# Kernel tuning notes

Hardware: AMD Instinct MI355X
Metric: run time of the kernel (lower is better)

Reference implementation:

```python
import jax, jax.numpy as jnp
import numpy as np

ALPHA = 1.0
N_OUTER, H_OUTER = 2, 0.5    # round(time_1/step_size_1) Euler steps of size step_size_1
N_INNER, H_INNER = 4, 0.25   # round(time_2/step_size_2) Euler steps inside each CGP


def _conv1x1(x, w, b):
    # x: [B,C,N,L], w: [O,C], b: [O] -> [B,O,N,L]  (1x1 Conv2d)
    return jnp.einsum('oc,bcnl->bonl', w, x) + b[None, :, None, None]


def _norm_adj(a):
    # row-normalized A + I
    a = a + jnp.eye(a.shape[0], dtype=a.dtype)
    return a / a.sum(axis=1, keepdims=True)


def _cgp(x, a_norm, w, b):
    # continuous graph propagation: dx/dt = alpha * (A_norm x - x), Euler integrated
    for _ in range(N_INNER):
        ax = jnp.einsum('nm,bcml->bcnl', a_norm, x)
        x = x + H_INNER * ALPHA * (ax - x)
    return _conv1x1(x, w, b)


def setup_inputs() -> dict:
    key = jax.random.key(0)
    ks = jax.random.split(key, 8)
    B, L, N, C_IN = 16, 12, 2000, 2
    C, E, C_OUT = 32, 128, 12

    def w(k, o, c, s=0.05):
        return jax.random.normal(k, (o, c), jnp.float32) * s

    return {
        'x': jax.random.normal(ks[0], (B, L, N, C_IN), jnp.float32),
        'adj': jax.random.uniform(ks[1], (N, N), jnp.float32),
        'w_start': w(ks[2], C, C_IN), 'b_start': jnp.zeros((C,), jnp.float32),
        'w_g1': w(ks[3], C, C), 'b_g1': jnp.zeros((C,), jnp.float32),
        'w_g2': w(ks[4], C, C), 'b_g2': jnp.zeros((C,), jnp.float32),
        'w_e0': w(ks[5], E // 2, C), 'b_e0': jnp.zeros((E // 2,), jnp.float32),
        'w_e1': w(ks[6], E, E // 2), 'b_e1': jnp.zeros((E,), jnp.float32),
        'w_e2': w(ks[7], C_OUT, E), 'b_e2': jnp.zeros((C_OUT,), jnp.float32),
    }


def reference(x, adj, w_start, b_start, w_g1, b_g1, w_g2, b_g2,
              w_e0, b_e0, w_e1, b_e1, w_e2, b_e2):
    # x: [B, L, N, C_in] -> channels-first [B, C_in, N, L]
    h = jnp.swapaxes(x, -1, -3)
    h = _conv1x1(h, w_start, b_start)
    a1 = _norm_adj(adj)
    a2 = _norm_adj(adj.T)
    # outer Euler ODE over STBlock (dropout = identity in eval mode)
    for _ in range(N_OUTER):
        h = h + H_OUTER * (_cgp(h, a1, w_g1, b_g1) + _cgp(h, a2, w_g2, b_g2))
    # layer_norm over all non-batch dims, no affine
    mu = h.mean(axis=(1, 2, 3), keepdims=True)
    var = h.var(axis=(1, 2, 3), keepdims=True)
    h = (h - mu) / jnp.sqrt(var + 1e-5)
    h = jax.nn.relu(_conv1x1(h, w_e0, b_e0))
    h = jax.nn.relu(_conv1x1(h, w_e1, b_e1))
    h = _conv1x1(h, w_e2, b_e2)
    return jnp.swapaxes(h, -1, -3)  # [B, L, N, out_channels]
```

## Files before the change

kernel.cpp:

```cpp
#include <hip/hip_runtime.h>
#include <math.h>

#define NN 2000
#define NP 2048
#define NB 16
#define NL 12
#define KW 6144
#define SW 384
#define LNCNT 768000.0f

#define O_ROWS ((size_t)0)
#define O_COLS ((size_t)2048)
#define O_LN   ((size_t)4096)
#define O_CM   ((size_t)4224)
#define O_CV   ((size_t)4672)
#define SZH ((size_t)2097152)
#define R1  ((size_t)8192)
#define R2  (R1 + 4*SZH)
#define R3  (R2 + 4*SZH)
#define O_X   (R3 + 0)
#define O_XTH (R3 + 768000)
#define O_XTL (O_XTH + 393216)
#define O_YF  (O_XTL + 393216)
#define O_YTH (O_YF + 1572864)
#define O_YTL (O_YTH + 786432)
#define O_ZF  (O_YTL + 786432)
#define O_H   R1

typedef __attribute__((ext_vector_type(8))) short short8;
typedef __attribute__((ext_vector_type(4))) float f32x4;

__device__ __forceinline__ unsigned short f2bf(float f) {
  union { float f; unsigned u; } x; x.f = f;
  unsigned r = x.u + 0x7fff + ((x.u >> 16) & 1);
  return (unsigned short)(r >> 16);
}
__device__ __forceinline__ float bf2f(unsigned short b) {
  union { unsigned u; float f; } x; x.u = ((unsigned)b) << 16;
  return x.f;
}
__device__ __forceinline__ void gld16(const void* g, void* l) {
  __builtin_amdgcn_global_load_lds(
      (const __attribute__((address_space(1))) unsigned int*)g,
      (__attribute__((address_space(3))) unsigned int*)l, 16, 0, 0);
}

__device__ __forceinline__ float blockReduceSum(float v, float* sbuf) {
  #pragma unroll
  for (int off = 32; off > 0; off >>= 1) v += __shfl_down(v, off, 64);
  int wid = threadIdx.x >> 6, lane = threadIdx.x & 63;
  if (lane == 0) sbuf[wid] = v;
  __syncthreads();
  v = (threadIdx.x < 4) ? sbuf[threadIdx.x] : 0.f;
  if (threadIdx.x < 64) { v += __shfl_down(v, 2, 64); v += __shfl_down(v, 1, 64); }
  return v;
}

__global__ void k_rowsum(const float* __restrict__ adj, float* __restrict__ rows) {
  __shared__ float sb[4];
  int n = blockIdx.x;
  const float4* a4 = (const float4*)(adj + (size_t)n * NN);
  float s = 0.f;
  for (int t = threadIdx.x; t < NN / 4; t += 256) {
    float4 v = a4[t];
    s += v.x + v.y + v.z + v.w;
  }
  s = blockReduceSum(s, sb);
  if (threadIdx.x == 0) rows[n] = s + 1.0f;
}

__global__ void k_colsum(const float* __restrict__ adj, float* __restrict__ cols) {
  __shared__ float sb[4][64];
  int col = blockIdx.x * 64 + (threadIdx.x & 63);
  int rg = threadIdx.x >> 6;
  float s = 0.f;
  if (col < NN)
    for (int m = rg; m < NN; m += 4) s += adj[(size_t)m * NN + col];
  sb[rg][threadIdx.x & 63] = s;
  __syncthreads();
  if (rg == 0 && col < NN)
    cols[col] = sb[0][threadIdx.x] + sb[1][threadIdx.x] + sb[2][threadIdx.x] + sb[3][threadIdx.x] + 1.0f;
}

__global__ void k_buildM8(const float* __restrict__ adj, const float* __restrict__ rows,
                          const float* __restrict__ cols,
                          unsigned short* __restrict__ M1h, unsigned short* __restrict__ M1l,
                          unsigned short* __restrict__ M2h, unsigned short* __restrict__ M2l,
                          unsigned short* __restrict__ M1Th, unsigned short* __restrict__ M1Tl,
                          unsigned short* __restrict__ M2Th, unsigned short* __restrict__ M2Tl) {
  __shared__ float Ta[64][65];
  __shared__ float Tb[64][65];
  int r0 = blockIdx.y * 64, c0 = blockIdx.x * 64;
  for (int e = threadIdx.x; e < 4096; e += 256) {
    int i = e >> 6, j = e & 63;
    int rr = r0 + i, cc = c0 + j;
    Ta[i][j] = (rr < NN && cc < NN) ? adj[(size_t)rr * NN + cc] : 0.f;
    int rr2 = c0 + i, cc2 = r0 + j;
    Tb[i][j] = (rr2 < NN && cc2 < NN) ? adj[(size_t)rr2 * NN + cc2] : 0.f;
  }
  __syncthreads();
  for (int e = threadIdx.x; e < 4096; e += 256) {
    int i = e >> 6, j = e & 63;
    int n = r0 + i, m = c0 + j;
    bool in = (n < NN && m < NN);
    float d = (n == m) ? 1.f : 0.f;
    float v1 = 0.f, v2 = 0.f, v1t = 0.f, v2t = 0.f;
    if (in) {
      v1  = 0.75f * d + 0.25f * (Ta[i][j] + d) / rows[n];
      v2  = 0.75f * d + 0.25f * (Tb[j][i] + d) / cols[n];
      v1t = 0.75f * d + 0.25f * (Tb[j][i] + d) / rows[m];
      v2t = 0.75f * d + 0.25f * (Ta[i][j] + d) / cols[m];
    }
    size_t o = (size_t)n * NP + m;
    unsigned short h;
    h = f2bf(v1);  M1h[o]  = h; M1l[o]  = f2bf(v1  - bf2f(h));
    h = f2bf(v2);  M2h[o]  = h; M2l[o]  = f2bf(v2  - bf2f(h));
    h = f2bf(v1t); M1Th[o] = h; M1Tl[o] = f2bf(v1t - bf2f(h));
    h = f2bf(v2t); M2Th[o] = h; M2Tl[o] = f2bf(v2t - bf2f(h));
  }
}

__global__ void k_prep(const float* __restrict__ wS, const float* __restrict__ bS,
                       const float* __restrict__ G1, const float* __restrict__ bg1,
                       const float* __restrict__ G2, const float* __restrict__ bg2,
                       float* __restrict__ Cm, float* __restrict__ cvec) {
  __shared__ float A1[64], A2[64], u1[32], v2[32];
  int t = threadIdx.x;
  int c = t >> 1, ci = t & 1;
  Cm[t] = wS[c * 2 + ci];
  float a1 = 0.f, a2 = 0.f;
  for (int j = 0; j < 32; ++j) {
    a1 += G1[c * 32 + j] * wS[j * 2 + ci];
    a2 += G2[c * 32 + j] * wS[j * 2 + ci];
  }
  A1[t] = a1; A2[t] = a2;
  Cm[64 + t] = a1;
  Cm[128 + t] = a2;
  __syncthreads();
  float b11 = 0, b12 = 0, b21 = 0, b22 = 0;
  for (int j = 0; j < 32; ++j) {
    b11 += G1[c * 32 + j] * A1[j * 2 + ci];
    b12 += G1[c * 32 + j] * A2[j * 2 + ci];
    b21 += G2[c * 32 + j] * A1[j * 2 + ci];
    b22 += G2[c * 32 + j] * A2[j * 2 + ci];
  }
  Cm[192 + t] = 0.25f * b11;
  Cm[256 + t] = 0.25f * b12;
  Cm[320 + t] = 0.25f * b21;
  Cm[384 + t] = 0.25f * b22;
  if (t < 32) {
    float uu = 0.f, vv = 0.f;
    for (int j = 0; j < 32; ++j) {
      float F = G1[t * 32 + j] + G2[t * 32 + j];
      uu += F * bS[j];
      vv += F * (bg1[j] + bg2[j]);
    }
    u1[t] = uu; v2[t] = vv;
  }
  __syncthreads();
  if (t < 32) {
    float u2v = 0.f;
    for (int j = 0; j < 32; ++j)
      u2v += (G1[t * 32 + j] + G2[t * 32 + j]) * u1[j];
    cvec[t] = bS[t] + u1[t] + 0.25f * u2v + (bg1[t] + bg2[t]) + 0.25f * v2[t];
  }
}

struct MG {
  const unsigned short *ah, *al, *bh, *bl;
  unsigned short *ch, *cl;
  float *cf;
};

template <int BN_, int OUTF32>
__global__ __launch_bounds__(256) void mgemm(MG g0, MG g1, int lda, int ldb,
                                             int ldc, int K) {
  MG g = (blockIdx.z == 0) ? g0 : g1;
  __shared__ __align__(16) unsigned short sAh[128 * 32];
  __shared__ __align__(16) unsigned short sAl[128 * 32];
  __shared__ __align__(16) unsigned short sBh[BN_ * 32];
  __shared__ __align__(16) unsigned short sBl[BN_ * 32];
  const int tid = threadIdx.x;
  const int wid = tid >> 6, lane = tid & 63;
  const int row0 = blockIdx.y * 128, col0 = blockIdx.x * BN_;
  const int FN = BN_ / 32;
  const int wr = (wid >> 1) * 64;
  const int wc = (wid & 1) * (BN_ / 2);
  const int lr = lane & 15;
  const int lk = (lane >> 4) * 8;
  const int r16 = lane >> 2;
  const int k16 = (lane & 3) * 8;
  const int BCH = BN_ / 16;
  const int CPW = (16 + 2 * BCH) / 4;

  f32x4 acc[4][FN];
  #pragma unroll
  for (int m = 0; m < 4; ++m)
    #pragma unroll
    for (int n = 0; n < FN; ++n) acc[m][n] = {0.f, 0.f, 0.f, 0.f};

  for (int k0 = 0; k0 < K; k0 += 32) {
    #pragma unroll
    for (int c = 0; c < CPW; ++c) {
      int gch = wid * CPW + c;
      const unsigned short* src;
      unsigned short* dst;
      if (gch < 16) {
        int q = gch & 7;
        src = (gch < 8 ? g.ah : g.al) + (size_t)(row0 + q * 16 + r16) * lda + k0 + k16;
        dst = (gch < 8 ? sAh : sAl) + q * 512;
      } else {
        int gb = gch - 16;
        int q = (gb < BCH) ? gb : gb - BCH;
        src = (gb < BCH ? g.bh : g.bl) + (size_t)(col0 + q * 16 + r16) * ldb + k0 + k16;
        dst = (gb < BCH ? sBh : sBl) + q * 512;
      }
      gld16(src, dst);
    }
    __syncthreads();
    short8 ahf[4], alf[4], bhf[FN], blf[FN];
    #pragma unroll
    for (int m = 0; m < 4; ++m) {
      ahf[m] = *(const short8*)&sAh[(wr + m * 16 + lr) * 32 + lk];
      alf[m] = *(const short8*)&sAl[(wr + m * 16 + lr) * 32 + lk];
    }
    #pragma unroll
    for (int n = 0; n < FN; ++n) {
      bhf[n] = *(const short8*)&sBh[(wc + n * 16 + lr) * 32 + lk];
      blf[n] = *(const short8*)&sBl[(wc + n * 16 + lr) * 32 + lk];
    }
    #pragma unroll
    for (int m = 0; m < 4; ++m)
      #pragma unroll
      for (int n = 0; n < FN; ++n) {
        acc[m][n] = __builtin_amdgcn_mfma_f32_16x16x32_bf16(ahf[m], bhf[n], acc[m][n], 0, 0, 0);
        acc[m][n] = __builtin_amdgcn_mfma_f32_16x16x32_bf16(ahf[m], blf[n], acc[m][n], 0, 0, 0);
        acc[m][n] = __builtin_amdgcn_mfma_f32_16x16x32_bf16(alf[m], bhf[n], acc[m][n], 0, 0, 0);
      }
    __syncthreads();
  }
  #pragma unroll
  for (int m = 0; m < 4; ++m)
    #pragma unroll
    for (int n = 0; n < FN; ++n)
      #pragma unroll
      for (int r = 0; r < 4; ++r) {
        int row = row0 + wr + m * 16 + (lane >> 4) * 4 + r;
        int col = col0 + wc + n * 16 + lr;
        float v = acc[m][n][r];
        if (OUTF32) {
          g.cf[(size_t)row * ldc + col] = v;
        } else {
          unsigned short h = f2bf(v);
          g.ch[(size_t)row * ldc + col] = h;
          g.cl[(size_t)row * ldc + col] = f2bf(v - bf2f(h));
        }
      }
}

__global__ void k_transpose(const unsigned short* __restrict__ S,
                            unsigned short* __restrict__ D) {
  const unsigned short* src = S + (size_t)blockIdx.z * 4194304;
  unsigned short* dst = D + (size_t)blockIdx.z * 4194304;
  __shared__ unsigned short t[64][72];
  int bx = blockIdx.x * 64, by = blockIdx.y * 64;
  int tid = threadIdx.x;
  int i0 = tid >> 4, j0 = (tid & 15) * 4;
  #pragma unroll
  for (int p = 0; p < 4; ++p) {
    int i = i0 + p * 16;
    ushort4 v = *(const ushort4*)&src[(size_t)(by + i) * NP + bx + j0];
    t[j0 + 0][i] = v.x; t[j0 + 1][i] = v.y; t[j0 + 2][i] = v.z; t[j0 + 3][i] = v.w;
  }
  __syncthreads();
  #pragma unroll
  for (int p = 0; p < 4; ++p) {
    int i = i0 + p * 16;
    ushort4 v;
    v.x = t[i][j0]; v.y = t[i][j0 + 1]; v.z = t[i][j0 + 2]; v.w = t[i][j0 + 3];
    *(ushort4*)&dst[(size_t)(bx + i) * NP + by + j0] = v;
  }
}

__global__ void k_buildX(const float* __restrict__ xin, float* __restrict__ X) {
  int idx = blockIdx.x * 256 + threadIdx.x;
  if (idx >= NN * SW) return;
  int n = idx / SW, p = idx % SW;
  int bl = p >> 1, ci = p & 1;
  X[idx] = xin[((size_t)bl * NN + n) * 2 + ci];
}

__global__ void k_buildXT(const float* __restrict__ xin,
                          unsigned short* __restrict__ XTh,
                          unsigned short* __restrict__ XTl) {
  int idx = blockIdx.x * 256 + threadIdx.x;
  if (idx >= SW * NP) return;
  int q = idx >> 11, n = idx & (NP - 1);
  float v = 0.f;
  if (n < NN) {
    int bl = q >> 1, ci = q & 1;
    v = xin[((size_t)bl * NN + n) * 2 + ci];
  }
  unsigned short h = f2bf(v);
  XTh[idx] = h; XTl[idx] = f2bf(v - bf2f(h));
}

__global__ void k_reshapeYT(const float* __restrict__ Yf,
                            unsigned short* __restrict__ YTh,
                            unsigned short* __restrict__ YTl) {
  __shared__ float t[64][65];
  int q0 = blockIdx.x * 64;
  int n0 = blockIdx.y * 64;
  int half = (q0 >= 384) ? 2048 : 0;
  int qs = (q0 >= 384) ? q0 - 384 : q0;
  int tid = threadIdx.x;
  int i0 = tid >> 4, j0 = (tid & 15) * 4;
  #pragma unroll
  for (int p = 0; p < 4; ++p) {
    int i = i0 + p * 16;
    float4 v = *(const float4*)&Yf[(size_t)(half + n0 + i) * SW + qs + j0];
    t[j0 + 0][i] = v.x; t[j0 + 1][i] = v.y; t[j0 + 2][i] = v.z; t[j0 + 3][i] = v.w;
  }
  __syncthreads();
  #pragma unroll
  for (int p = 0; p < 4; ++p) {
    int i = i0 + p * 16;
    #pragma unroll
    for (int j = 0; j < 4; ++j) {
      float v = t[i][j0 + j];
      size_t o = (size_t)(q0 + i) * NP + n0 + j0 + j;
      unsigned short h = f2bf(v);
      YTh[o] = h; YTl[o] = f2bf(v - bf2f(h));
    }
  }
}

__global__ void k_combine(const float* __restrict__ X, const float* __restrict__ Yf,
                          const float* __restrict__ Zf, const float* __restrict__ Cm,
                          const float* __restrict__ cvec, float* __restrict__ H) {
  int idx = blockIdx.x * 256 + threadIdx.x;
  if (idx >= NN * KW) return;
  int n = idx / KW, j = idx % KW;
  int b = j / 384, r = j % 384;
  int l = r >> 5, c = r & 31;
  int p2 = (b * NL + l) * 2;
  int c2 = c * 2;
  size_t pX  = (size_t)n * SW + p2;
  size_t pY2 = (size_t)(2048 + n) * SW + p2;
  size_t pZ1 = (size_t)n * 768 + p2;
  size_t pZ2 = (size_t)(2048 + n) * 768 + p2;
  float acc = cvec[c];
  acc += Cm[c2] * X[pX] + Cm[c2 + 1] * X[pX + 1];
  acc += Cm[64 + c2] * Yf[pX] + Cm[64 + c2 + 1] * Yf[pX + 1];
  acc += Cm[128 + c2] * Yf[pY2] + Cm[128 + c2 + 1] * Yf[pY2 + 1];
  acc += Cm[192 + c2] * Zf[pZ1] + Cm[192 + c2 + 1] * Zf[pZ1 + 1];
  acc += Cm[256 + c2] * Zf[pZ1 + 384] + Cm[256 + c2 + 1] * Zf[pZ1 + 385];
  acc += Cm[320 + c2] * Zf[pZ2] + Cm[320 + c2 + 1] * Zf[pZ2 + 1];
  acc += Cm[384 + c2] * Zf[pZ2 + 384] + Cm[384 + c2 + 1] * Zf[pZ2 + 385];
  H[idx] = acc;
}

__global__ void k_lnreduce(const float* __restrict__ H, float* __restrict__ ln) {
  __shared__ float sb[4];
  int b = blockIdx.x & 15, chunk = blockIdx.x >> 4;
  int n0 = chunk * 125;
  float s = 0.f, ss = 0.f;
  for (int t = threadIdx.x; t < 125 * 96; t += 256) {
    int n = n0 + t / 96, q = t % 96;
    float4 v = *(const float4*)(H + (size_t)n * KW + b * 384 + q * 4);
    s += v.x + v.y + v.z + v.w;
    ss += v.x * v.x + v.y * v.y + v.z * v.z + v.w * v.w;
  }
  s = blockReduceSum(s, sb);
  __syncthreads();
  ss = blockReduceSum(ss, sb);
  if (threadIdx.x == 0) { atomicAdd(&ln[b], s); atomicAdd(&ln[16 + b], ss); }
}

__global__ __launch_bounds__(256, 2) void k_epilogue(
    const float* __restrict__ H, const float* __restrict__ ln,
    const float* __restrict__ w0, const float* __restrict__ b0,
    const float* __restrict__ w1, const float* __restrict__ b1,
    const float* __restrict__ w2, const float* __restrict__ b2,
    float* __restrict__ out) {
  int p = blockIdx.x * 256 + threadIdx.x;
  if (p >= NB * NL * NN) return;
  int b = p / (NL * NN);
  int r = p % (NL * NN);
  int l = r / NN;
  int n = r % NN;
  float mu = ln[b] * (1.0f / LNCNT);
  float var = ln[16 + b] * (1.0f / LNCNT) - mu * mu;
  float rs = rsqrtf(fmaxf(var, 0.f) + 1e-5f);
  float x[32];
  const float* hp = H + (size_t)n * KW + b * 384 + l * 32;
  #pragma unroll
  for (int q = 0; q < 8; ++q) {
    float4 v = *(const float4*)(hp + q * 4);
    x[q * 4 + 0] = (v.x - mu) * rs;
    x[q * 4 + 1] = (v.y - mu) * rs;
    x[q * 4 + 2] = (v.z - mu) * rs;
    x[q * 4 + 3] = (v.w - mu) * rs;
  }
  float y0[64];
  #pragma unroll
  for (int o = 0; o < 64; ++o) {
    float acc = b0[o];
    const float* wr = w0 + o * 32;
    #pragma unroll
    for (int i = 0; i < 32; ++i) acc += wr[i] * x[i];
    y0[o] = fmaxf(acc, 0.f);
  }
  float outv[12];
  #pragma unroll
  for (int o = 0; o < 12; ++o) outv[o] = b2[o];
  for (int jj = 0; jj < 128; ++jj) {
    float acc = b1[jj];
    const float* wr = w1 + jj * 64;
    #pragma unroll
    for (int i = 0; i < 64; ++i) acc += wr[i] * y0[i];
    acc = fmaxf(acc, 0.f);
    #pragma unroll
    for (int o = 0; o < 12; ++o) outv[o] += w2[o * 128 + jj] * acc;
  }
  float* op = out + ((size_t)(b * NL + l) * NN + n) * 12;
  #pragma unroll
  for (int o = 0; o < 12; ++o) op[o] = outv[o];
}

extern "C" void kernel_launch(void* const* d_in, const int* in_sizes, int n_in,
                              void* d_out, int out_size, void* d_ws, size_t ws_size,
                              hipStream_t stream) {
  (void)in_sizes; (void)n_in; (void)out_size; (void)ws_size;
  const float* x   = (const float*)d_in[0];
  const float* adj = (const float*)d_in[1];
  const float* wS  = (const float*)d_in[2];
  const float* bS  = (const float*)d_in[3];
  const float* G1  = (const float*)d_in[4];
  const float* bg1 = (const float*)d_in[5];
  const float* G2  = (const float*)d_in[6];
  const float* bg2 = (const float*)d_in[7];
  const float* we0 = (const float*)d_in[8];
  const float* be0 = (const float*)d_in[9];
  const float* we1 = (const float*)d_in[10];
  const float* be1 = (const float*)d_in[11];
  const float* we2 = (const float*)d_in[12];
  const float* be2 = (const float*)d_in[13];
  float* out = (float*)d_out;
  float* wsf = (float*)d_ws;

  float* rows = wsf + O_ROWS;
  float* cols = wsf + O_COLS;
  float* lnb  = wsf + O_LN;
  float* Cm   = wsf + O_CM;
  float* cvec = wsf + O_CV;

  unsigned short* M1h  = (unsigned short*)(wsf + R1);
  unsigned short* M1l  = (unsigned short*)(wsf + R1 + SZH);
  unsigned short* M2h  = (unsigned short*)(wsf + R1 + 2 * SZH);
  unsigned short* M2l  = (unsigned short*)(wsf + R1 + 3 * SZH);
  unsigned short* M1Th = (unsigned short*)(wsf + R2);
  unsigned short* M1Tl = (unsigned short*)(wsf + R2 + SZH);
  unsigned short* M2Th = (unsigned short*)(wsf + R2 + 2 * SZH);
  unsigned short* M2Tl = (unsigned short*)(wsf + R2 + 3 * SZH);
  unsigned short* T1h  = (unsigned short*)(wsf + R3);
  unsigned short* T1l  = (unsigned short*)(wsf + R3 + SZH);
  unsigned short* T2h  = (unsigned short*)(wsf + R3 + 2 * SZH);
  unsigned short* T2l  = (unsigned short*)(wsf + R3 + 3 * SZH);
  unsigned short* T1Th = M1Th;
  unsigned short* T1Tl = M1Tl;
  unsigned short* T2Th = M2Th;
  unsigned short* T2Tl = M2Tl;
  unsigned short* Phi  = (unsigned short*)(wsf + R1);
  unsigned short* Plo  = (unsigned short*)(wsf + R1 + 2 * SZH);
  float* X   = wsf + O_X;
  unsigned short* XTh = (unsigned short*)(wsf + O_XTH);
  unsigned short* XTl = (unsigned short*)(wsf + O_XTL);
  float* Yf  = wsf + O_YF;
  unsigned short* YTh = (unsigned short*)(wsf + O_YTH);
  unsigned short* YTl = (unsigned short*)(wsf + O_YTL);
  float* Zf  = wsf + O_ZF;
  float* H   = wsf + O_H;

  hipMemsetAsync(lnb, 0, 32 * sizeof(float), stream);
  k_rowsum<<<NN, 256, 0, stream>>>(adj, rows);
  k_colsum<<<32, 256, 0, stream>>>(adj, cols);
  k_buildM8<<<dim3(32, 32), 256, 0, stream>>>(adj, rows, cols,
      M1h, M1l, M2h, M2l, M1Th, M1Tl, M2Th, M2Tl);
  k_prep<<<1, 64, 0, stream>>>(wS, bS, G1, bg1, G2, bg2, Cm, cvec);

  {
    MG a0 = {M1h, M1l, M1Th, M1Tl, T1h, T1l, nullptr};
    MG a1 = {M2h, M2l, M2Th, M2Tl, T2h, T2l, nullptr};
    mgemm<128, 0><<<dim3(16, 16, 2), 256, 0, stream>>>(a0, a1, NP, NP, NP, NP);
  }
  k_transpose<<<dim3(32, 32, 4), 256, 0, stream>>>(T1h, T1Th);
  {
    MG b0 = {T1h, T1l, T1Th, T1Tl, Phi, Plo, nullptr};
    MG b1 = {T2h, T2l, T2Th, T2Tl, Phi + (size_t)NP * NP, Plo + (size_t)NP * NP, nullptr};
    mgemm<128, 0><<<dim3(16, 16, 2), 256, 0, stream>>>(b0, b1, NP, NP, NP, NP);
  }
  k_buildX<<<(NN * SW + 255) / 256, 256, 0, stream>>>(x, X);
  k_buildXT<<<(SW * NP + 255) / 256, 256, 0, stream>>>(x, XTh, XTl);
  {
    MG c0 = {Phi, Plo, XTh, XTl, nullptr, nullptr, Yf};
    mgemm<64, 1><<<dim3(6, 32, 1), 256, 0, stream>>>(c0, c0, NP, NP, SW, NP);
  }
  k_reshapeYT<<<dim3(12, 32), 256, 0, stream>>>(Yf, YTh, YTl);
  {
    MG e0 = {Phi, Plo, YTh, YTl, nullptr, nullptr, Zf};
    mgemm<64, 1><<<dim3(12, 32, 1), 256, 0, stream>>>(e0, e0, NP, NP, 768, NP);
  }

  k_combine<<<(NN * KW + 255) / 256, 256, 0, stream>>>(X, Yf, Zf, Cm, cvec, H);
  k_lnreduce<<<256, 256, 0, stream>>>(H, lnb);
  k_epilogue<<<(NB * NL * NN + 255) / 256, 256, 0, stream>>>(
      H, lnb, we0, be0, we1, be1, we2, be2, out);
}
```

Measured before the change: 862.6 us.

## Rewrite epilogue MLP on MFMA with split-bf16 weights staged in LDS

Replaces the per-thread scalar FP32 three-layer epilogue MLP with a block-tiled version. Each wave processes 16 nodes, runs the layers as bf16 MFMA using hi/lo split (three products) to approximate FP32 precision, and stages intermediate activations in LDS. The goal is to remove the heavy scalar FMA work and register pressure of the old per-point kernel. In exchange it adds weight conversion per block, extra LDS traffic and barriers, and a slight precision loss from the split-bf16 scheme.

```diff
diff --git a/kernel.cpp b/kernel.cpp
--- a/kernel.cpp
+++ b/kernel.cpp
@@ -377,55 +377,182 @@
   if (threadIdx.x == 0) { atomicAdd(&ln[b], s); atomicAdd(&ln[16 + b], ss); }
 }
 
-__global__ __launch_bounds__(256, 2) void k_epilogue(
+__global__ __launch_bounds__(256) void k_epilogue_mfma(
     const float* __restrict__ H, const float* __restrict__ ln,
     const float* __restrict__ w0, const float* __restrict__ b0,
     const float* __restrict__ w1, const float* __restrict__ b1,
     const float* __restrict__ w2, const float* __restrict__ b2,
     float* __restrict__ out) {
-  int p = blockIdx.x * 256 + threadIdx.x;
-  if (p >= NB * NL * NN) return;
-  int b = p / (NL * NN);
-  int r = p % (NL * NN);
-  int l = r / NN;
-  int n = r % NN;
-  float mu = ln[b] * (1.0f / LNCNT);
-  float var = ln[16 + b] * (1.0f / LNCNT) - mu * mu;
-  float rs = rsqrtf(fmaxf(var, 0.f) + 1e-5f);
-  float x[32];
-  const float* hp = H + (size_t)n * KW + b * 384 + l * 32;
-  #pragma unroll
-  for (int q = 0; q < 8; ++q) {
-    float4 v = *(const float4*)(hp + q * 4);
-    x[q * 4 + 0] = (v.x - mu) * rs;
-    x[q * 4 + 1] = (v.y - mu) * rs;
-    x[q * 4 + 2] = (v.z - mu) * rs;
-    x[q * 4 + 3] = (v.w - mu) * rs;
-  }
-  float y0[64];
-  #pragma unroll
-  for (int o = 0; o < 64; ++o) {
-    float acc = b0[o];
-    const float* wr = w0 + o * 32;
-    #pragma unroll
-    for (int i = 0; i < 32; ++i) acc += wr[i] * x[i];
-    y0[o] = fmaxf(acc, 0.f);
-  }
-  float outv[12];
-  #pragma unroll
-  for (int o = 0; o < 12; ++o) outv[o] = b2[o];
-  for (int jj = 0; jj < 128; ++jj) {
-    float acc = b1[jj];
-    const float* wr = w1 + jj * 64;
-    #pragma unroll
-    for (int i = 0; i < 64; ++i) acc += wr[i] * y0[i];
-    acc = fmaxf(acc, 0.f);
-    #pragma unroll
-    for (int o = 0; o < 12; ++o) outv[o] += w2[o * 128 + jj] * acc;
-  }
-  float* op = out + ((size_t)(b * NL + l) * NN + n) * 12;
-  #pragma unroll
-  for (int o = 0; o < 12; ++o) op[o] = outv[o];
+  __shared__ __align__(16) unsigned short sW0h[64 * 40], sW0l[64 * 40];
+  __shared__ __align__(16) unsigned short sW1h[128 * 72], sW1l[128 * 72];
+  __shared__ __align__(16) unsigned short sW2h[16 * 136], sW2l[16 * 136];
+  __shared__ __align__(16) unsigned short sY0h[4 * 16 * 72], sY0l[4 * 16 * 72];
+  __shared__ __align__(16) unsigned short sY1h[4 * 16 * 136], sY1l[4 * 16 * 136];
+  __shared__ float b0s[64], b1s[128];
+  const int tid = threadIdx.x;
+
+  {
+    int t0 = tid * 8, r = t0 >> 5, c = t0 & 31;
+    float4 a = *(const float4*)(w0 + t0);
+    float4 bq = *(const float4*)(w0 + t0 + 4);
+    float v[8] = {a.x, a.y, a.z, a.w, bq.x, bq.y, bq.z, bq.w};
+    short8 vh, vl;
+    #pragma unroll
+    for (int j = 0; j < 8; ++j) {
+      unsigned short h = f2bf(v[j]);
+      vh[j] = (short)h; vl[j] = (short)f2bf(v[j] - bf2f(h));
+    }
+    *(short8*)&sW0h[r * 40 + c] = vh;
+    *(short8*)&sW0l[r * 40 + c] = vl;
+  }
+  #pragma unroll
+  for (int q = 0; q < 4; ++q) {
+    int idx = tid * 32 + q * 8, r = idx >> 6, c = idx & 63;
+    float4 a = *(const float4*)(w1 + idx);
+    float4 bq = *(const float4*)(w1 + idx + 4);
+    float v[8] = {a.x, a.y, a.z, a.w, bq.x, bq.y, bq.z, bq.w};
+    short8 vh, vl;
+    #pragma unroll
+    for (int j = 0; j < 8; ++j) {
+      unsigned short h = f2bf(v[j]);
+      vh[j] = (short)h; vl[j] = (short)f2bf(v[j] - bf2f(h));
+    }
+    *(short8*)&sW1h[r * 72 + c] = vh;
+    *(short8*)&sW1l[r * 72 + c] = vl;
+  }
+  {
+    int idx = tid * 8, r = idx >> 7, c = idx & 127;
+    float v[8] = {0, 0, 0, 0, 0, 0, 0, 0};
+    if (r < 12) {
+      float4 a = *(const float4*)(w2 + r * 128 + c);
+      float4 bq = *(const float4*)(w2 + r * 128 + c + 4);
+      v[0] = a.x; v[1] = a.y; v[2] = a.z; v[3] = a.w;
+      v[4] = bq.x; v[5] = bq.y; v[6] = bq.z; v[7] = bq.w;
+    }
+    short8 vh, vl;
+    #pragma unroll
+    for (int j = 0; j < 8; ++j) {
+      unsigned short h = f2bf(v[j]);
+      vh[j] = (short)h; vl[j] = (short)f2bf(v[j] - bf2f(h));
+    }
+    *(short8*)&sW2h[r * 136 + c] = vh;
+    *(short8*)&sW2l[r * 136 + c] = vl;
+  }
+  if (tid < 64) b0s[tid] = b0[tid];
+  if (tid < 128) b1s[tid] = b1[tid];
+  __syncthreads();
+
+  const int wid = tid >> 6, lane = tid & 63;
+  const int lr = lane & 15, hk = lane >> 4;
+  const int lk = hk * 8;
+  const int bl = blockIdx.y, bb = bl / 12, ll = bl % 12;
+  const int ntile = blockIdx.x * 64 + wid * 16;
+
+  const float mu = ln[bb] * (1.0f / LNCNT);
+  const float var = ln[16 + bb] * (1.0f / LNCNT) - mu * mu;
+  const float rs = rsqrtf(fmaxf(var, 0.f) + 1e-5f);
+
+  short8 ah = {0, 0, 0, 0, 0, 0, 0, 0}, al = ah;
+  {
+    int n_row = ntile + lr;
+    if (n_row < NN) {
+      const float* hp = H + (size_t)n_row * KW + bb * 384 + ll * 32 + lk;
+      float4 v0 = *(const float4*)hp;
+      float4 v1 = *(const float4*)(hp + 4);
+      float xs[8] = {v0.x, v0.y, v0.z, v0.w, v1.x, v1.y, v1.z, v1.w};
+      #pragma unroll
+      for (int j = 0; j < 8; ++j) {
+        float xv = (xs[j] - mu) * rs;
+        unsigned short h = f2bf(xv);
+        ah[j] = (short)h; al[j] = (short)f2bf(xv - bf2f(h));
+      }
+    }
+  }
+
+  const int y0b = wid * 16 * 72;
+  {
+    f32x4 acc0[4];
+    #pragma unroll
+    for (int nf = 0; nf < 4; ++nf) {
+      short8 bh = *(const short8*)&sW0h[(nf * 16 + lr) * 40 + lk];
+      short8 bo = *(const short8*)&sW0l[(nf * 16 + lr) * 40 + lk];
+      f32x4 a = {0.f, 0.f, 0.f, 0.f};
+      a = __builtin_amdgcn_mfma_f32_16x16x32_bf16(ah, bh, a, 0, 0, 0);
+      a = __builtin_amdgcn_mfma_f32_16x16x32_bf16(ah, bo, a, 0, 0, 0);
+      a = __builtin_amdgcn_mfma_f32_16x16x32_bf16(al, bh, a, 0, 0, 0);
+      acc0[nf] = a;
+    }
+    #pragma unroll
+    for (int nf = 0; nf < 4; ++nf)
+      #pragma unroll
+      for (int r = 0; r < 4; ++r) {
+        int row = hk * 4 + r, col = nf * 16 + lr;
+        float v = fmaxf(acc0[nf][r] + b0s[col], 0.f);
+        unsigned short h = f2bf(v);
+        sY0h[y0b + row * 72 + col] = h;
+        sY0l[y0b + row * 72 + col] = f2bf(v - bf2f(h));
+      }
+  }
+  __syncthreads();
+
+  const int y1b = wid * 16 * 136;
+  {
+    short8 a1h[2], a1l[2];
+    #pragma unroll
+    for (int kc = 0; kc < 2; ++kc) {
+      a1h[kc] = *(const short8*)&sY0h[y0b + lr * 72 + kc * 32 + lk];
+      a1l[kc] = *(const short8*)&sY0l[y0b + lr * 72 + kc * 32 + lk];
+    }
+    f32x4 acc1[8];
+    #pragma unroll
+    for (int nf = 0; nf < 8; ++nf) {
+      f32x4 a = {0.f, 0.f, 0.f, 0.f};
+      #pragma unroll
+      for (int kc = 0; kc < 2; ++kc) {
+        short8 bh = *(const short8*)&sW1h[(nf * 16 + lr) * 72 + kc * 32 + lk];
+        short8 bo = *(const short8*)&sW1l[(nf * 16 + lr) * 72 + kc * 32 + lk];
+        a = __builtin_amdgcn_mfma_f32_16x16x32_bf16(a1h[kc], bh, a, 0, 0, 0);
+        a = __builtin_amdgcn_mfma_f32_16x16x32_bf16(a1h[kc], bo, a, 0, 0, 0);
+        a = __builtin_amdgcn_mfma_f32_16x16x32_bf16(a1l[kc], bh, a, 0, 0, 0);
+      }
+      acc1[nf] = a;
+    }
+    #pragma unroll
+    for (int nf = 0; nf < 8; ++nf)
+      #pragma unroll
+      for (int r = 0; r < 4; ++r) {
+        int row = hk * 4 + r, col = nf * 16 + lr;
+        float v = fmaxf(acc1[nf][r] + b1s[col], 0.f);
+        unsigned short h = f2bf(v);
+        sY1h[y1b + row * 136 + col] = h;
+        sY1l[y1b + row * 136 + col] = f2bf(v - bf2f(h));
+      }
+  }
+  __syncthreads();
+
+  {
+    f32x4 a2 = {0.f, 0.f, 0.f, 0.f};
+    #pragma unroll
+    for (int kc = 0; kc < 4; ++kc) {
+      short8 a2h = *(const short8*)&sY1h[y1b + lr * 136 + kc * 32 + lk];
+      short8 a2l = *(const short8*)&sY1l[y1b + lr * 136 + kc * 32 + lk];
+      short8 bh = *(const short8*)&sW2h[lr * 136 + kc * 32 + lk];
+      short8 bo = *(const short8*)&sW2l[lr * 136 + kc * 32 + lk];
+      a2 = __builtin_amdgcn_mfma_f32_16x16x32_bf16(a2h, bh, a2, 0, 0, 0);
+      a2 = __builtin_amdgcn_mfma_f32_16x16x32_bf16(a2h, bo, a2, 0, 0, 0);
+      a2 = __builtin_amdgcn_mfma_f32_16x16x32_bf16(a2l, bh, a2, 0, 0, 0);
+    }
+    int o = lr;
+    if (o < 12) {
+      float bv = b2[o];
+      #pragma unroll
+      for (int r = 0; r < 4; ++r) {
+        int n = ntile + hk * 4 + r;
+        if (n < NN)
+          out[((size_t)(bb * NL + ll) * NN + n) * 12 + o] = a2[r] + bv;
+      }
+    }
+  }
 }
 
 extern "C" void kernel_launch(void* const* d_in, const int* in_sizes, int n_in,
@@ -514,6 +641,6 @@
 
   k_combine<<<(NN * KW + 255) / 256, 256, 0, stream>>>(X, Yf, Zf, Cm, cvec, H);
   k_lnreduce<<<256, 256, 0, stream>>>(H, lnb);
-  k_epilogue<<<(NB * NL * NN + 255) / 256, 256, 0, stream>>>(
+  k_epilogue_mfma<<<dim3(32, NB * NL), 256, 0, stream>>>(
       H, lnb, we0, be0, we1, be1, we2, be2, out);
 }
```

After: 859.2 us. Within noise of the previous version (-0.4%).
